# Kernel optimization log

Measured on AMD Instinct MI355X. Metric: run time of the kernel, lower is better.

## Reference

```python
import jax, jax.numpy as jnp
import numpy as np

B, N, DIM = 4, 1024, 1024
H, D = 16, 64          # num_heads, head_dim
SW = 256               # sliding_window
ROPE_BASE = 10000.0
LN_EPS = 1e-5


def _layernorm(x, w, b):
    mu = jnp.mean(x, axis=-1, keepdims=True)
    var = jnp.mean((x - mu) ** 2, axis=-1, keepdims=True)
    return (x - mu) * jax.lax.rsqrt(var + LN_EPS) * w + b


def _rotate_half(x):
    x1, x2 = jnp.split(x, 2, axis=-1)
    return jnp.concatenate([-x2, x1], axis=-1)


def setup_inputs() -> dict:
    key = jax.random.key(0)
    ks = jax.random.split(key, 8)
    s = 0.02
    return {
        "x": jax.random.normal(ks[0], (B, N, DIM), dtype=jnp.float32),
        "qkv_w": jax.random.normal(ks[1], (3 * H * D, DIM), dtype=jnp.float32) * s,
        "qn_w": jnp.ones((D,), jnp.float32),
        "qn_b": jnp.zeros((D,), jnp.float32),
        "kn_w": jnp.ones((D,), jnp.float32),
        "kn_b": jnp.zeros((D,), jnp.float32),
        "sinks": jax.random.normal(ks[2], (H,), dtype=jnp.float32),
        "proj_w": jax.random.normal(ks[3], (DIM, H * D), dtype=jnp.float32) * s,
        "proj_b": jnp.zeros((DIM,), jnp.float32),
    }


def reference(x, qkv_w, qn_w, qn_b, kn_w, kn_b, sinks, proj_w, proj_b):
    Bx, Nx, _ = x.shape
    # fused QKV projection -> [3, B, H, N, D]
    qkv = (x @ qkv_w.T).reshape(Bx, Nx, 3, H, D).transpose(2, 0, 3, 1, 4)
    q, k, v = qkv[0], qkv[1], qkv[2]
    # qk-norm (LayerNorm over head_dim)
    q = _layernorm(q, qn_w, qn_b)
    k = _layernorm(k, kn_w, kn_b)
    # 1d RoPE (DeepseekV3-style: emb = cat(freqs, freqs), rotate_half)
    inv_freq = 1.0 / (ROPE_BASE ** (jnp.arange(0, D, 2, dtype=jnp.float32) / D))
    freqs = jnp.arange(Nx, dtype=jnp.float32)[:, None] * inv_freq[None, :]  # [N, D/2]
    emb = jnp.concatenate([freqs, freqs], axis=-1)                           # [N, D]
    cos, sin = jnp.cos(emb), jnp.sin(emb)
    q = q * cos + _rotate_half(q) * sin
    k = k * cos + _rotate_half(k) * sin
    # sliding-window causal mask with attention sinks
    sm_scale = 1.0 / np.sqrt(D)
    scores = jnp.einsum("bhqd,bhkd->bhqk", q, k) * sm_scale  # [B,H,N,N]
    i = jnp.arange(Nx)[:, None]
    j = jnp.arange(Nx)[None, :]
    allowed = (j <= i) & (j > i - SW)
    scores = jnp.where(allowed, scores, -jnp.inf)
    # append sink logit per head, softmax, drop sink column
    sink_col = jnp.broadcast_to(sinks[None, :, None, None], (Bx, H, Nx, 1))
    logits = jnp.concatenate([scores, sink_col], axis=-1)
    probs = jax.nn.softmax(logits, axis=-1)[..., :-1]
    out = jnp.einsum("bhqk,bhkd->bhqd", probs, v)
    out = out.transpose(0, 2, 1, 3).reshape(Bx, Nx, H * D)
    return out @ proj_w.T + proj_b
```

## Files before the change

### kernel.cpp

```cpp
#include <hip/hip_runtime.h>
#include <stdint.h>

typedef unsigned short u16;
typedef __bf16 bf16x8 __attribute__((ext_vector_type(8)));
typedef float f32x4 __attribute__((ext_vector_type(4)));

__device__ __forceinline__ float b2f(u16 u) {
  union { uint32_t i; float f; } x; x.i = ((uint32_t)u) << 16; return x.f;
}
__device__ __forceinline__ u16 f2b(float f) {
  union { float f; uint32_t i; } x; x.f = f;
  uint32_t r = x.i + 0x7fffu + ((x.i >> 16) & 1u);
  return (u16)(r >> 16);
}
__device__ __forceinline__ uint4 pk8(const float4 a, const float4 b) {
  uint4 r;
  r.x = (uint32_t)f2b(a.x) | ((uint32_t)f2b(a.y) << 16);
  r.y = (uint32_t)f2b(a.z) | ((uint32_t)f2b(a.w) << 16);
  r.z = (uint32_t)f2b(b.x) | ((uint32_t)f2b(b.y) << 16);
  r.w = (uint32_t)f2b(b.z) | ((uint32_t)f2b(b.w) << 16);
  return r;
}
__device__ __forceinline__ void gload_lds16(const u16* g, u16* l) {
  __builtin_amdgcn_global_load_lds(
      (const __attribute__((address_space(1))) void*)g,
      (__attribute__((address_space(3))) void*)l, 16, 0, 0);
}

__launch_bounds__(256)
__global__ void prep(const float* __restrict__ x, const float* __restrict__ wq,
                     const float* __restrict__ wp, u16* __restrict__ dst,
                     float* __restrict__ tab) {
  if (blockIdx.x >= 4096) {
    const int tid = (blockIdx.x - 4096) * 256 + threadIdx.x;
    const int pos = tid >> 5, idx = tid & 31;
    const float f = pos * exp2f(idx * -0.41524101186092029f);
    float s, c;
    sincosf(f, &s, &c);
    *(float2*)(tab + tid * 2) = make_float2(c, s);
    return;
  }
  const int i = (blockIdx.x * 256 + threadIdx.x) * 8;
  const float* src; int local, base;
  if (i < 4194304)      { src = x;  local = i;           base = 0; }
  else if (i < 7340032) { src = wq; local = i - 4194304; base = 4194304; }
  else                  { src = wp; local = i - 7340032; base = 7340032; }
  const int row = local >> 10, col = local & 1023;
  const int slot = ((col >> 3) & 7) ^ (row & 7);
  const float4 a = *(const float4*)(src + local);
  const float4 b = *(const float4*)(src + local + 4);
  *(uint4*)(dst + base + row * 1024 + (col & ~63) + slot * 8) = pk8(a, b);
}

template<int MODE>
__launch_bounds__(256)
__global__ void gemm128(const u16* __restrict__ A, const u16* __restrict__ Bw,
                        void* __restrict__ Cp, const float* __restrict__ bias,
                        const float* __restrict__ qn_w, const float* __restrict__ qn_b,
                        const float* __restrict__ kn_w, const float* __restrict__ kn_b,
                        const float* __restrict__ tab, int K) {
  __shared__ __align__(16) u16 As[128 * 64];
  __shared__ __align__(16) u16 Bs[128 * 64];
  const int t = threadIdx.x;
  const int w = t >> 6, l = t & 63, lr = l & 15, lg = l >> 4;
  const int m0 = blockIdx.y * 128, n0 = blockIdx.x * 128;
  const int wm = (w >> 1) * 64, wn = (w & 1) * 64;
  const int srow = w * 32 + (l >> 3);
  const int scol = (l & 7) * 8;
  const u16* gA = A  + (m0 + srow) * K + scol;
  const u16* gB = Bw + (n0 + srow) * K + scol;

  f32x4 acc[4][4] = {};
  const int nk = K >> 6;
  for (int kt = 0; kt < nk; ++kt) {
    const int ko = kt * 64;
    __syncthreads();
#pragma unroll
    for (int i = 0; i < 4; ++i)
      gload_lds16(gA + i * 8 * K + ko, As + (w * 32 + i * 8) * 64);
#pragma unroll
    for (int i = 0; i < 4; ++i)
      gload_lds16(gB + i * 8 * K + ko, Bs + (w * 32 + i * 8) * 64);
    __syncthreads();
    bf16x8 af0[4], af1[4], bf0[4], bf1[4];
#pragma unroll
    for (int i = 0; i < 4; ++i) {
      const int ra = wm + i * 16 + lr;
      const int sa = (lg ^ (ra & 7)) * 8;
      af0[i] = *(const bf16x8*)(As + ra * 64 + sa);
      af1[i] = *(const bf16x8*)(As + ra * 64 + (sa ^ 32));
    }
#pragma unroll
    for (int j = 0; j < 4; ++j) {
      const int rb = wn + j * 16 + lr;
      const int sb = (lg ^ (rb & 7)) * 8;
      bf0[j] = *(const bf16x8*)(Bs + rb * 64 + sb);
      bf1[j] = *(const bf16x8*)(Bs + rb * 64 + (sb ^ 32));
    }
#pragma unroll
    for (int i = 0; i < 4; ++i)
#pragma unroll
      for (int j = 0; j < 4; ++j) {
        acc[i][j] = __builtin_amdgcn_mfma_f32_16x16x32_bf16(af0[i], bf0[j], acc[i][j], 0, 0, 0);
        acc[i][j] = __builtin_amdgcn_mfma_f32_16x16x32_bf16(af1[i], bf1[j], acc[i][j], 0, 0, 0);
      }
  }

  if (MODE == 1) {
#pragma unroll
    for (int i = 0; i < 4; ++i)
#pragma unroll
      for (int j = 0; j < 4; ++j)
#pragma unroll
        for (int r = 0; r < 4; ++r) {
          const int gm = m0 + wm + i * 16 + lg * 4 + r;
          const int gn = n0 + wn + j * 16 + lr;
          ((float*)Cp)[(gm << 10) + gn] = acc[i][j][r] + bias[gn];
        }
    return;
  }
  const int whichB = blockIdx.x >> 3;
  const int hh = ((n0 + wn) >> 6) & 15;
  u16* Cb = (u16*)Cp + whichB * 4194304;
  if (whichB == 2) {
#pragma unroll
    for (int i = 0; i < 4; ++i)
#pragma unroll
      for (int j = 0; j < 4; ++j)
#pragma unroll
        for (int r = 0; r < 4; ++r) {
          const int gm = m0 + wm + i * 16 + lg * 4 + r;
          Cb[(((gm >> 10) * 16 + hh) << 16) + ((gm & 1023) << 6) + j * 16 + lr] =
              f2b(acc[i][j][r]);
        }
    return;
  }
  const float* wl = whichB ? kn_w : qn_w;
  const float* bl = whichB ? kn_b : qn_b;
  float wln[4], bln[4];
#pragma unroll
  for (int j = 0; j < 4; ++j) { wln[j] = wl[j * 16 + lr]; bln[j] = bl[j * 16 + lr]; }
#pragma unroll
  for (int i = 0; i < 4; ++i)
#pragma unroll
    for (int r = 0; r < 4; ++r) {
      const int gm = m0 + wm + i * 16 + lg * 4 + r;
      const int pos = gm & 1023;
      float v0 = acc[i][0][r], v1 = acc[i][1][r], v2 = acc[i][2][r], v3 = acc[i][3][r];
      float s = v0 + v1 + v2 + v3;
#pragma unroll
      for (int m = 1; m < 16; m <<= 1) s += __shfl_xor(s, m);
      const float mu = s * 0.015625f;
      const float d0 = v0 - mu, d1 = v1 - mu, d2 = v2 - mu, d3 = v3 - mu;
      float qv = d0 * d0 + d1 * d1 + d2 * d2 + d3 * d3;
#pragma unroll
      for (int m = 1; m < 16; m <<= 1) qv += __shfl_xor(qv, m);
      const float rstd = rsqrtf(qv * 0.015625f + 1e-5f);
      float nn[4];
      nn[0] = d0 * rstd * wln[0] + bln[0];
      nn[1] = d1 * rstd * wln[1] + bln[1];
      nn[2] = d2 * rstd * wln[2] + bln[2];
      nn[3] = d3 * rstd * wln[3] + bln[3];
      const float2 csA = *(const float2*)(tab + (pos * 32 + lr) * 2);
      const float2 csB = *(const float2*)(tab + (pos * 32 + 16 + lr) * 2);
      float o[4];
      o[0] = nn[0] * csA.x - nn[2] * csA.y;
      o[1] = nn[1] * csB.x - nn[3] * csB.y;
      o[2] = nn[2] * csA.x + nn[0] * csA.y;
      o[3] = nn[3] * csB.x + nn[1] * csB.y;
      u16* cb = Cb + (((gm >> 10) * 16 + hh) << 16) + (pos << 6);
      if (whichB == 1) {
        const int key = pos & 7;
#pragma unroll
        for (int j = 0; j < 4; ++j) {
          const int d = j * 16 + lr;
          cb[((d >> 3) ^ key) * 8 + (d & 7)] = f2b(o[j]);
        }
      } else {
#pragma unroll
        for (int j = 0; j < 4; ++j) cb[j * 16 + lr] = f2b(o[j]);
      }
    }
}

__launch_bounds__(256)
__global__ void vtrans(const u16* __restrict__ v, u16* __restrict__ vt) {
  __shared__ u16 tile[128 * 65];
  const int t = threadIdx.x;
  const int bh = blockIdx.x >> 3;
  const int n0 = (blockIdx.x & 7) * 128;
  const u16* src = v + bh * 65536 + n0 * 64;
#pragma unroll
  for (int it = 0; it < 8; ++it) {
    const int e = (it * 256 + t) * 4;
    const int n = e >> 6, d = e & 63;
    const ushort4 x = *(const ushort4*)(src + n * 64 + d);
    tile[n * 65 + d + 0] = x.x;
    tile[n * 65 + d + 1] = x.y;
    tile[n * 65 + d + 2] = x.z;
    tile[n * 65 + d + 3] = x.w;
  }
  __syncthreads();
  u16* dst = vt + bh * 65536;
#pragma unroll
  for (int it = 0; it < 8; ++it) {
    const int o = (it * 256 + t) * 4;
    const int d = o >> 7, c = o & 127;
    ushort4 y;
    y.x = tile[(c + 0) * 65 + d];
    y.y = tile[(c + 1) * 65 + d];
    y.z = tile[(c + 2) * 65 + d];
    y.w = tile[(c + 3) * 65 + d];
    const int gj = n0 + c;
    const int nb = gj >> 6, jl = gj & 63;
    const int slot = (jl >> 3) ^ (d & 7);
    *(ushort4*)(dst + nb * 4096 + d * 64 + slot * 8 + (jl & 7)) = y;
  }
}

__launch_bounds__(256, 2)
__global__ void attn_kernel(const u16* __restrict__ q, const u16* __restrict__ k,
                            const u16* __restrict__ vt, const float* __restrict__ sinks,
                            u16* __restrict__ ao) {
  __shared__ __align__(16) u16 Ks[20480];
  __shared__ __align__(16) u16 Vs[20480];
  const int t = threadIdx.x, w = t >> 6, l = t & 63, lr = l & 15, lg = l >> 4;
  const int bid = blockIdx.x;
  const int qb = bid & 15, h = (bid >> 4) & 15, b = bid >> 8;
  const int i0 = qb * 64 + w * 16;
  const int bh = b * 16 + h;
  const u16* qp = q + bh * 65536;
  const u16* kp = k + bh * 65536;
  const u16* vp = vt + bh * 65536;
  const int j0 = qb * 64 - 256;

#pragma unroll
  for (int i = 0; i < 10; ++i) {
    const int c = w * 10 + i;
    int off = j0 * 64 + c * 512 + l * 8;
    off = off < 0 ? 0 : off;
    gload_lds16(kp + off, Ks + c * 512);
  }
#pragma unroll
  for (int i = 0; i < 10; ++i) {
    const int c = w * 10 + i;
    const int n = c >> 3, p = c & 7;
    int nb = qb - 4 + n;
    nb = nb < 0 ? 0 : nb;
    gload_lds16(vp + nb * 4096 + p * 512 + l * 8, Vs + c * 512);
  }
  const bf16x8 qf0 = *(const bf16x8*)(qp + (i0 + lr) * 64 + lg * 8);
  const bf16x8 qf1 = *(const bf16x8*)(qp + (i0 + lr) * 64 + 32 + lg * 8);
  __syncthreads();

  const int key = lr & 7;
  f32x4 sacc[17];
#pragma unroll
  for (int jt = 0; jt < 17; ++jt) {
    const int r = w * 16 + jt * 16 + lr;
    const bf16x8 kf0 = *(const bf16x8*)(Ks + r * 64 + ((lg ^ key)) * 8);
    const bf16x8 kf1 = *(const bf16x8*)(Ks + r * 64 + (((lg + 4) ^ key)) * 8);
    f32x4 a = {0.f, 0.f, 0.f, 0.f};
    a = __builtin_amdgcn_mfma_f32_16x16x32_bf16(qf0, kf0, a, 0, 0, 0);
    a = __builtin_amdgcn_mfma_f32_16x16x32_bf16(qf1, kf1, a, 0, 0, 0);
    sacc[jt] = a;
  }
  const float sink = sinks[h];
  const int ja = i0 - 256;
  float mx[4] = {-1e30f, -1e30f, -1e30f, -1e30f};
#pragma unroll
  for (int jt = 0; jt < 17; ++jt)
#pragma unroll
    for (int r = 0; r < 4; ++r) {
      const int qi = i0 + lg * 4 + r;
      const int jg = ja + jt * 16 + lr;
      const bool ok = (jg >= 0) && (jg <= qi) && (jg > qi - 256);
      const float sv = ok ? sacc[jt][r] * 0.125f : -1e30f;
      sacc[jt][r] = sv;
      mx[r] = fmaxf(mx[r], sv);
    }
#pragma unroll
  for (int off = 1; off < 16; off <<= 1)
#pragma unroll
    for (int r = 0; r < 4; ++r) mx[r] = fmaxf(mx[r], __shfl_xor(mx[r], off));
#pragma unroll
  for (int r = 0; r < 4; ++r) mx[r] = fmaxf(mx[r], sink);
  float sum[4] = {0.f, 0.f, 0.f, 0.f};
#pragma unroll
  for (int jt = 0; jt < 17; ++jt)
#pragma unroll
    for (int r = 0; r < 4; ++r) {
      const float e = __expf(sacc[jt][r] - mx[r]);
      sacc[jt][r] = e;
      sum[r] += e;
    }
#pragma unroll
  for (int off = 1; off < 16; off <<= 1)
#pragma unroll
    for (int r = 0; r < 4; ++r) sum[r] += __shfl_xor(sum[r], off);
  float inv[4];
#pragma unroll
  for (int r = 0; r < 4; ++r) inv[r] = 1.0f / (sum[r] + __expf(sink - mx[r]));

  __syncthreads();
  u16* pb = Ks + w * 4736;
  {
    ushort4 z; z.x = 0; z.y = 0; z.z = 0; z.w = 0;
    *(ushort4*)(pb + (l >> 2) * 296 + 272 + (l & 3) * 4) = z;
  }
#pragma unroll
  for (int jt = 0; jt < 17; ++jt)
#pragma unroll
    for (int r = 0; r < 4; ++r)
      pb[(lg * 4 + r) * 296 + jt * 16 + lr] = f2b(sacc[jt][r] * inv[r]);

  f32x4 oacc[4] = {};
#pragma unroll
  for (int ks = 0; ks < 9; ++ks) {
    const bf16x8 pf = *(const bf16x8*)(pb + lr * 296 + ks * 32 + lg * 8);
#pragma unroll
    for (int dt = 0; dt < 4; ++dt) {
      int r = w * 16 + ks * 32 + lg * 8;
      r = r < 320 ? r : 0;
      const int n = r >> 6, jl = r & 63;
      const int slot = (jl >> 3) ^ (lr & 7);
      const bf16x8 vf = *(const bf16x8*)(Vs + n * 4096 + (dt * 16 + lr) * 64 + slot * 8);
      oacc[dt] = __builtin_amdgcn_mfma_f32_16x16x32_bf16(pf, vf, oacc[dt], 0, 0, 0);
    }
  }
#pragma unroll
  for (int dt = 0; dt < 4; ++dt)
#pragma unroll
    for (int r = 0; r < 4; ++r) {
      const int m = (b << 10) + i0 + lg * 4 + r;
      const int cg = (dt * 2 + (lr >> 3)) ^ (m & 7);
      ao[(m << 10) + (h << 6) + cg * 8 + (lr & 7)] = f2b(oacc[dt][r]);
    }
}

extern "C" void kernel_launch(void* const* d_in, const int* in_sizes, int n_in,
                              void* d_out, int out_size, void* d_ws, size_t ws_size,
                              hipStream_t stream) {
  const float* x      = (const float*)d_in[0];
  const float* qkv_w  = (const float*)d_in[1];
  const float* qn_w   = (const float*)d_in[2];
  const float* qn_b   = (const float*)d_in[3];
  const float* kn_w   = (const float*)d_in[4];
  const float* kn_b   = (const float*)d_in[5];
  const float* sinks  = (const float*)d_in[6];
  const float* proj_w = (const float*)d_in[7];
  const float* proj_b = (const float*)d_in[8];
  float* out = (float*)d_out;
  u16* ws     = (u16*)d_ws;
  u16* qkv    = ws;
  u16* xb     = ws + 12582912;
  u16* wprojb = ws + 19922944;
  float* tab  = (float*)(ws + 20971520);
  u16* ao     = ws + 21233664;
  u16* vtw    = ws + 12582912;

  prep<<<4224, 256, 0, stream>>>(x, qkv_w, proj_w, xb, tab);
  gemm128<0><<<dim3(24, 32), 256, 0, stream>>>(xb, xb + 4194304, qkv, nullptr,
                                               qn_w, qn_b, kn_w, kn_b, tab, 1024);
  vtrans<<<512, 256, 0, stream>>>(qkv + 8388608, vtw);
  attn_kernel<<<1024, 256, 0, stream>>>(qkv, qkv + 4194304, vtw, sinks, ao);
  gemm128<1><<<dim3(8, 32), 256, 0, stream>>>(ao, wprojb, out, proj_b,
                                              nullptr, nullptr, nullptr, nullptr,
                                              nullptr, 1024);
}
```

Before: 199.7 us.

## Fuse V transpose into QKV GEMM, shrink K-tile, split proj GEMM tiles

```diff
diff --git a/kernel.cpp b/kernel.cpp
--- a/kernel.cpp
+++ b/kernel.cpp
@@ -46,67 +46,65 @@
   else if (i < 7340032) { src = wq; local = i - 4194304; base = 4194304; }
   else                  { src = wp; local = i - 7340032; base = 7340032; }
   const int row = local >> 10, col = local & 1023;
-  const int slot = ((col >> 3) & 7) ^ (row & 7);
+  const int slot = ((col >> 3) & 3) ^ (row & 3);
   const float4 a = *(const float4*)(src + local);
   const float4 b = *(const float4*)(src + local + 4);
-  *(uint4*)(dst + base + row * 1024 + (col & ~63) + slot * 8) = pk8(a, b);
-}
-
-template<int MODE>
+  *(uint4*)(dst + base + (row << 10) + (col & ~31) + (slot << 3)) = pk8(a, b);
+}
+
 __launch_bounds__(256)
-__global__ void gemm128(const u16* __restrict__ A, const u16* __restrict__ Bw,
-                        void* __restrict__ Cp, const float* __restrict__ bias,
-                        const float* __restrict__ qn_w, const float* __restrict__ qn_b,
-                        const float* __restrict__ kn_w, const float* __restrict__ kn_b,
-                        const float* __restrict__ tab, int K) {
-  __shared__ __align__(16) u16 As[128 * 64];
-  __shared__ __align__(16) u16 Bs[128 * 64];
+__global__ void gemm_qkv(const u16* __restrict__ A, const u16* __restrict__ Bw,
+                         u16* __restrict__ Cp, u16* __restrict__ vt,
+                         const float* __restrict__ qn_w, const float* __restrict__ qn_b,
+                         const float* __restrict__ kn_w, const float* __restrict__ kn_b,
+                         const float* __restrict__ tab, int K) {
+  __shared__ __align__(16) u16 As[128 * 32];
+  __shared__ __align__(16) u16 Bs[128 * 32];
   const int t = threadIdx.x;
   const int w = t >> 6, l = t & 63, lr = l & 15, lg = l >> 4;
   const int m0 = blockIdx.y * 128, n0 = blockIdx.x * 128;
   const int wm = (w >> 1) * 64, wn = (w & 1) * 64;
-  const int srow = w * 32 + (l >> 3);
-  const int scol = (l & 7) * 8;
-  const u16* gA = A  + (m0 + srow) * K + scol;
-  const u16* gB = Bw + (n0 + srow) * K + scol;
+  const int srow = w * 32 + (l >> 2);
+  const int scol = (l & 3) * 8;
+  const u16* ga0 = A  + (m0 + srow) * K + scol;
+  const u16* ga1 = ga0 + 16 * K;
+  const u16* gb0 = Bw + (n0 + srow) * K + scol;
+  const u16* gb1 = gb0 + 16 * K;
+  u16* la0 = As + w * 1024;
+  u16* la1 = As + w * 1024 + 512;
+  u16* lb0 = Bs + w * 1024;
+  u16* lb1 = Bs + w * 1024 + 512;
 
   f32x4 acc[4][4] = {};
-  const int nk = K >> 6;
+  const int nk = K >> 5;
   for (int kt = 0; kt < nk; ++kt) {
-    const int ko = kt * 64;
+    const int ko = kt * 32;
     __syncthreads();
-#pragma unroll
-    for (int i = 0; i < 4; ++i)
-      gload_lds16(gA + i * 8 * K + ko, As + (w * 32 + i * 8) * 64);
-#pragma unroll
-    for (int i = 0; i < 4; ++i)
-      gload_lds16(gB + i * 8 * K + ko, Bs + (w * 32 + i * 8) * 64);
+    gload_lds16(ga0 + ko, la0);
+    gload_lds16(ga1 + ko, la1);
+    gload_lds16(gb0 + ko, lb0);
+    gload_lds16(gb1 + ko, lb1);
     __syncthreads();
-    bf16x8 af0[4], af1[4], bf0[4], bf1[4];
+    bf16x8 af[4], bfr[4];
 #pragma unroll
     for (int i = 0; i < 4; ++i) {
       const int ra = wm + i * 16 + lr;
-      const int sa = (lg ^ (ra & 7)) * 8;
-      af0[i] = *(const bf16x8*)(As + ra * 64 + sa);
-      af1[i] = *(const bf16x8*)(As + ra * 64 + (sa ^ 32));
+      af[i] = *(const bf16x8*)(As + ra * 32 + ((lg ^ (ra & 3)) << 3));
     }
 #pragma unroll
     for (int j = 0; j < 4; ++j) {
       const int rb = wn + j * 16 + lr;
-      const int sb = (lg ^ (rb & 7)) * 8;
-      bf0[j] = *(const bf16x8*)(Bs + rb * 64 + sb);
-      bf1[j] = *(const bf16x8*)(Bs + rb * 64 + (sb ^ 32));
+      bfr[j] = *(const bf16x8*)(Bs + rb * 32 + ((lg ^ (rb & 3)) << 3));
     }
 #pragma unroll
     for (int i = 0; i < 4; ++i)
 #pragma unroll
-      for (int j = 0; j < 4; ++j) {
-        acc[i][j] = __builtin_amdgcn_mfma_f32_16x16x32_bf16(af0[i], bf0[j], acc[i][j], 0, 0, 0);
-        acc[i][j] = __builtin_amdgcn_mfma_f32_16x16x32_bf16(af1[i], bf1[j], acc[i][j], 0, 0, 0);
-      }
-  }
-
-  if (MODE == 1) {
+      for (int j = 0; j < 4; ++j)
+        acc[i][j] = __builtin_amdgcn_mfma_f32_16x16x32_bf16(af[i], bfr[j], acc[i][j], 0, 0, 0);
+  }
+  const int whichB = blockIdx.x >> 3;
+  const int hh = ((n0 + wn) >> 6) & 15;
+  if (whichB == 2) {
 #pragma unroll
     for (int i = 0; i < 4; ++i)
 #pragma unroll
@@ -114,23 +112,10 @@
 #pragma unroll
         for (int r = 0; r < 4; ++r) {
           const int gm = m0 + wm + i * 16 + lg * 4 + r;
-          const int gn = n0 + wn + j * 16 + lr;
-          ((float*)Cp)[(gm << 10) + gn] = acc[i][j][r] + bias[gn];
-        }
-    return;
-  }
-  const int whichB = blockIdx.x >> 3;
-  const int hh = ((n0 + wn) >> 6) & 15;
-  u16* Cb = (u16*)Cp + whichB * 4194304;
-  if (whichB == 2) {
-#pragma unroll
-    for (int i = 0; i < 4; ++i)
-#pragma unroll
-      for (int j = 0; j < 4; ++j)
-#pragma unroll
-        for (int r = 0; r < 4; ++r) {
-          const int gm = m0 + wm + i * 16 + lg * 4 + r;
-          Cb[(((gm >> 10) * 16 + hh) << 16) + ((gm & 1023) << 6) + j * 16 + lr] =
+          const int bh = (gm >> 10) * 16 + hh;
+          const int pos = gm & 1023, nb = pos >> 6, jl = pos & 63;
+          const int d = j * 16 + lr;
+          vt[bh * 65536 + nb * 4096 + d * 64 + (((jl >> 3) ^ (d & 7)) << 3) + (jl & 7)] =
               f2b(acc[i][j][r]);
         }
     return;
@@ -140,6 +125,7 @@
   float wln[4], bln[4];
 #pragma unroll
   for (int j = 0; j < 4; ++j) { wln[j] = wl[j * 16 + lr]; bln[j] = bl[j * 16 + lr]; }
+  u16* Cb = Cp + whichB * 4194304;
 #pragma unroll
   for (int i = 0; i < 4; ++i)
 #pragma unroll
@@ -184,38 +170,61 @@
 }
 
 __launch_bounds__(256)
-__global__ void vtrans(const u16* __restrict__ v, u16* __restrict__ vt) {
-  __shared__ u16 tile[128 * 65];
+__global__ void gemm_proj(const u16* __restrict__ A, const u16* __restrict__ Bw,
+                          float* __restrict__ out, const float* __restrict__ bias,
+                          int K) {
+  __shared__ __align__(16) u16 As[128 * 32];
+  __shared__ __align__(16) u16 Bs[64 * 32];
   const int t = threadIdx.x;
-  const int bh = blockIdx.x >> 3;
-  const int n0 = (blockIdx.x & 7) * 128;
-  const u16* src = v + bh * 65536 + n0 * 64;
-#pragma unroll
-  for (int it = 0; it < 8; ++it) {
-    const int e = (it * 256 + t) * 4;
-    const int n = e >> 6, d = e & 63;
-    const ushort4 x = *(const ushort4*)(src + n * 64 + d);
-    tile[n * 65 + d + 0] = x.x;
-    tile[n * 65 + d + 1] = x.y;
-    tile[n * 65 + d + 2] = x.z;
-    tile[n * 65 + d + 3] = x.w;
-  }
-  __syncthreads();
-  u16* dst = vt + bh * 65536;
-#pragma unroll
-  for (int it = 0; it < 8; ++it) {
-    const int o = (it * 256 + t) * 4;
-    const int d = o >> 7, c = o & 127;
-    ushort4 y;
-    y.x = tile[(c + 0) * 65 + d];
-    y.y = tile[(c + 1) * 65 + d];
-    y.z = tile[(c + 2) * 65 + d];
-    y.w = tile[(c + 3) * 65 + d];
-    const int gj = n0 + c;
-    const int nb = gj >> 6, jl = gj & 63;
-    const int slot = (jl >> 3) ^ (d & 7);
-    *(ushort4*)(dst + nb * 4096 + d * 64 + slot * 8 + (jl & 7)) = y;
-  }
+  const int w = t >> 6, l = t & 63, lr = l & 15, lg = l >> 4;
+  const int m0 = blockIdx.y * 128, n0 = blockIdx.x * 64;
+  const int wm = (w >> 1) * 64, wn = (w & 1) * 32;
+  const int srowA = w * 32 + (l >> 2);
+  const int srowB = w * 16 + (l >> 2);
+  const int scol = (l & 3) * 8;
+  const u16* ga0 = A  + (m0 + srowA) * K + scol;
+  const u16* ga1 = ga0 + 16 * K;
+  const u16* gb  = Bw + (n0 + srowB) * K + scol;
+  u16* la0 = As + w * 1024;
+  u16* la1 = As + w * 1024 + 512;
+  u16* lb  = Bs + w * 512;
+
+  f32x4 acc[4][2] = {};
+  const int nk = K >> 5;
+  for (int kt = 0; kt < nk; ++kt) {
+    const int ko = kt * 32;
+    __syncthreads();
+    gload_lds16(ga0 + ko, la0);
+    gload_lds16(ga1 + ko, la1);
+    gload_lds16(gb + ko, lb);
+    __syncthreads();
+    bf16x8 af[4], bfr[2];
+#pragma unroll
+    for (int i = 0; i < 4; ++i) {
+      const int ra = wm + i * 16 + lr;
+      af[i] = *(const bf16x8*)(As + ra * 32 + ((lg ^ (ra & 3)) << 3));
+    }
+#pragma unroll
+    for (int j = 0; j < 2; ++j) {
+      const int rb = wn + j * 16 + lr;
+      bfr[j] = *(const bf16x8*)(Bs + rb * 32 + ((lg ^ (rb & 3)) << 3));
+    }
+#pragma unroll
+    for (int i = 0; i < 4; ++i)
+#pragma unroll
+      for (int j = 0; j < 2; ++j)
+        acc[i][j] = __builtin_amdgcn_mfma_f32_16x16x32_bf16(af[i], bfr[j], acc[i][j], 0, 0, 0);
+  }
+#pragma unroll
+  for (int i = 0; i < 4; ++i)
+#pragma unroll
+    for (int j = 0; j < 2; ++j)
+#pragma unroll
+      for (int r = 0; r < 4; ++r) {
+        const int gm = m0 + wm + i * 16 + lg * 4 + r;
+        const int gn = n0 + wn + j * 16 + lr;
+        out[(gm << 10) + gn] = acc[i][j][r] + bias[gn];
+      }
 }
 
 __launch_bounds__(256, 2)
@@ -333,8 +342,9 @@
 #pragma unroll
     for (int r = 0; r < 4; ++r) {
       const int m = (b << 10) + i0 + lg * 4 + r;
-      const int cg = (dt * 2 + (lr >> 3)) ^ (m & 7);
-      ao[(m << 10) + (h << 6) + cg * 8 + (lr & 7)] = f2b(oacc[dt][r]);
+      const int d = dt * 16 + lr;
+      const int cg = ((d >> 3) & 3) ^ (m & 3);
+      ao[(m << 10) + (h << 6) + (d & ~31) + (cg << 3) + (d & 7)] = f2b(oacc[dt][r]);
     }
 }
 
@@ -353,18 +363,15 @@
   float* out = (float*)d_out;
   u16* ws     = (u16*)d_ws;
   u16* qkv    = ws;
+  u16* vtw    = ws + 8388608;
   u16* xb     = ws + 12582912;
   u16* wprojb = ws + 19922944;
   float* tab  = (float*)(ws + 20971520);
   u16* ao     = ws + 21233664;
-  u16* vtw    = ws + 12582912;
 
   prep<<<4224, 256, 0, stream>>>(x, qkv_w, proj_w, xb, tab);
-  gemm128<0><<<dim3(24, 32), 256, 0, stream>>>(xb, xb + 4194304, qkv, nullptr,
-                                               qn_w, qn_b, kn_w, kn_b, tab, 1024);
-  vtrans<<<512, 256, 0, stream>>>(qkv + 8388608, vtw);
+  gemm_qkv<<<dim3(24, 32), 256, 0, stream>>>(xb, xb + 4194304, qkv, vtw,
+                                             qn_w, qn_b, kn_w, kn_b, tab, 1024);
   attn_kernel<<<1024, 256, 0, stream>>>(qkv, qkv + 4194304, vtw, sinks, ao);
-  gemm128<1><<<dim3(8, 32), 256, 0, stream>>>(ao, wprojb, out, proj_b,
-                                              nullptr, nullptr, nullptr, nullptr,
-                                              nullptr, 1024);
-}
+  gemm_proj<<<dim3(16, 32), 256, 0, stream>>>(ao, wprojb, out, proj_b, 1024);
+}
```

Result: no change. 200.8 us (+0.6%).
